# Kernel tuning notes

Measured on AMD Instinct MI355X. Metric: run time of the kernel, lower is better.

## Reference

```python
import jax, jax.numpy as jnp
import numpy as np

B, N, DIM = 32, 577, 768   # N = num_patches + 1
H, DH = 12, 64             # heads, dim_head; inner_dim = H*DH = 768
NEG = -987654321.0         # LSA diagonal mask value from the source


def setup_inputs() -> dict:
    key = jax.random.key(0)
    ks = jax.random.split(key, 5)
    inner = H * DH
    base_scale = DH ** -0.5
    return {
        "x": jax.random.normal(ks[0], (B, N, DIM), dtype=jnp.float32),
        "W_qkv": jax.random.normal(ks[1], (DIM, inner * 3), dtype=jnp.float32) * (DIM ** -0.5),
        "scale": base_scale * (1.0 + 0.01 * jax.random.normal(ks[2], (H,), dtype=jnp.float32)),
        "W_out": jax.random.normal(ks[3], (inner, DIM), dtype=jnp.float32) * (inner ** -0.5),
        "b_out": jnp.zeros((DIM,), dtype=jnp.float32),
    }


def reference(x, W_qkv, scale, W_out, b_out):
    b, n, _ = x.shape
    qkv = x @ W_qkv                                   # [b, n, 3*H*DH]
    q, k, v = jnp.split(qkv, 3, axis=-1)
    to_heads = lambda t: t.reshape(b, n, H, DH).transpose(0, 2, 1, 3)  # b h n d
    q, k, v = to_heads(q), to_heads(k), to_heads(v)
    # per-head learnable scale (LSA)
    dots = jnp.einsum('bhid,bhjd->bhij', q, k) * scale[None, :, None, None]
    # mask self-attention diagonal (eye scatter in the torch source)
    eye = jnp.eye(n, dtype=bool)
    dots = jnp.where(eye[None, None], NEG, dots)
    attn = jax.nn.softmax(dots, axis=-1)
    out = jnp.einsum('bhij,bhjd->bhid', attn, v)      # b h n d
    out = out.transpose(0, 2, 1, 3).reshape(b, n, H * DH)
    return out @ W_out + b_out
```

## Files before the change

kernel.cpp:

```cpp
#include <hip/hip_runtime.h>


typedef _Float16 half8  __attribute__((ext_vector_type(8)));
typedef _Float16 h4f    __attribute__((ext_vector_type(4)));
typedef __fp16   hv2    __attribute__((ext_vector_type(2)));
typedef __fp16   hv4    __attribute__((ext_vector_type(4)));
typedef float    floatx4 __attribute__((ext_vector_type(4)));

#define MTOT   18464
#define NEG_V  (-987654321.0f)
#define VTS    584

__device__ __forceinline__ void gl_lds16(const _Float16* g, _Float16* l) {
    __builtin_amdgcn_global_load_lds(
        (const __attribute__((address_space(1))) unsigned int*)g,
        (__attribute__((address_space(3))) unsigned int*)l,
        16, 0, 0);
}

__global__ __launch_bounds__(256) void cvt_x(const float* __restrict__ x,
                                             _Float16* __restrict__ x16) {
    const size_t idx = ((size_t)blockIdx.x * 256 + threadIdx.x) * 8;
    half8 h = {};
    if (idx < (size_t)MTOT * 768) {
        float4 a = *(const float4*)(x + idx);
        float4 b = *(const float4*)(x + idx + 4);
        h[0] = (_Float16)a.x; h[1] = (_Float16)a.y;
        h[2] = (_Float16)a.z; h[3] = (_Float16)a.w;
        h[4] = (_Float16)b.x; h[5] = (_Float16)b.y;
        h[6] = (_Float16)b.z; h[7] = (_Float16)b.w;
    }
    *(half8*)(x16 + idx) = h;
}

__global__ __launch_bounds__(256) void transpose_w(const float* __restrict__ src,
                                                   _Float16* __restrict__ dst,
                                                   int K, int Ncol) {
    __shared__ float tile[32][33];
    const int n0 = blockIdx.x * 32, k0 = blockIdx.y * 32;
    const int tx = threadIdx.x & 31, ty = threadIdx.x >> 5;
    for (int i = 0; i < 32; i += 8)
        tile[ty + i][tx] = src[(size_t)(k0 + ty + i) * Ncol + (n0 + tx)];
    __syncthreads();
    for (int i = 0; i < 32; i += 8)
        dst[(size_t)(n0 + ty + i) * K + (k0 + tx)] = (_Float16)tile[tx][ty + i];
}

__global__ __launch_bounds__(512, 4) void gemm_qkv(const _Float16* __restrict__ x16,
                                                   const _Float16* __restrict__ wT,
                                                   const float* __restrict__ scale,
                                                   _Float16* __restrict__ qg,
                                                   _Float16* __restrict__ kg,
                                                   _Float16* __restrict__ vT) {
    __shared__ _Float16 As[2][128 * 32];
    __shared__ _Float16 Bs[2][256 * 32];
    const unsigned orig = blockIdx.x;
    const unsigned xcd = orig & 7u, bidx = orig >> 3;
    const unsigned swz = (xcd == 0u ? 0u : 164u + (xcd - 1u) * 163u) + bidx;
    const unsigned mi = swz / 9u, ni = swz - mi * 9u;
    const int m0 = (int)mi * 128, n0 = (int)ni * 256;
    const int tid = threadIdx.x;
    const int lane = tid & 63, wv = tid >> 6;
    const int wrow = wv >> 2, wcol = wv & 3;
    const int lr = lane & 15, lq = lane >> 4;

    const int ra  = tid >> 2,         ca  = (((tid & 3) ^ ((ra  >> 1) & 3)) * 8);
    const int rb0 = tid >> 2,         cb0 = (((tid & 3) ^ ((rb0 >> 1) & 3)) * 8);
    const int rb1 = (512 + tid) >> 2, cb1 = (((tid & 3) ^ ((rb1 >> 1) & 3)) * 8);
    const int xc = (lq ^ ((lr >> 1) & 3)) * 8;

    floatx4 acc[4][4];
    const floatx4 fz = {0.f, 0.f, 0.f, 0.f};
    for (int i = 0; i < 4; ++i)
        for (int j = 0; j < 4; ++j) acc[i][j] = fz;

    #define STAGE_QKV(ki, bfx)                                                     \
        do {                                                                       \
            const int kk_ = (ki) * 32;                                             \
            gl_lds16(x16 + (size_t)(m0 + ra) * 768 + kk_ + ca, &As[bfx][wv*64*8]); \
            gl_lds16(wT + (size_t)(n0 + rb0) * 768 + kk_ + cb0, &Bs[bfx][wv*64*8]);\
            gl_lds16(wT + (size_t)(n0 + rb1) * 768 + kk_ + cb1,                    \
                     &Bs[bfx][(512 + wv*64) * 8]);                                 \
        } while (0)

    STAGE_QKV(0, 0);
    for (int ki = 0; ki < 24; ++ki) {
        const int bf = ki & 1;
        if (ki < 23) {
            STAGE_QKV(ki + 1, bf ^ 1);
            asm volatile("s_waitcnt vmcnt(3)" ::: "memory");
        } else {
            asm volatile("s_waitcnt vmcnt(0)" ::: "memory");
        }
        asm volatile("s_barrier" ::: "memory");

        half8 af[4], bfr[4];
        #pragma unroll
        for (int i = 0; i < 4; ++i)
            af[i] = *(const half8*)&As[bf][(wrow * 64 + i * 16 + lr) * 32 + xc];
        #pragma unroll
        for (int j = 0; j < 4; ++j)
            bfr[j] = *(const half8*)&Bs[bf][(wcol * 64 + j * 16 + lr) * 32 + xc];
        #pragma unroll
        for (int i = 0; i < 4; ++i)
            #pragma unroll
            for (int j = 0; j < 4; ++j)
                acc[i][j] = __builtin_amdgcn_mfma_f32_16x16x32_f16(af[i], bfr[j], acc[i][j], 0, 0, 0);

        asm volatile("s_waitcnt lgkmcnt(0)\n\ts_barrier" ::: "memory");
    }
    #undef STAGE_QKV

    const int cbase = n0 + wcol * 64;
    const int which = cbase / 768;
    const int h = (cbase - which * 768) >> 6;
    const float qsc = (which == 0) ? scale[h] * 1.4426950408889634f : 1.0f;
    #pragma unroll
    for (int j = 0; j < 4; ++j) {
        const int d = j * 16 + lr;
        #pragma unroll
        for (int i = 0; i < 4; ++i)
            #pragma unroll
            for (int r = 0; r < 4; ++r) {
                const int row = m0 + wrow * 64 + i * 16 + lq * 4 + r;
                if (row >= MTOT) continue;
                const unsigned bb = (unsigned)row / 577u;
                const unsigned nn = (unsigned)row - bb * 577u;
                const _Float16 val = (_Float16)(acc[i][j][r] * qsc);
                const size_t head = (size_t)(bb * 12 + h);
                if (which == 0)      qg[(head * 577 + nn) * 64 + d] = val;
                else if (which == 1) kg[(head * 577 + nn) * 64 + d] = val;
                else                 vT[(head * 64 + d) * VTS + nn] = val;
            }
    }
}

__global__ __launch_bounds__(256) void attn_kernel(const _Float16* __restrict__ qg,
                                                   const _Float16* __restrict__ kg,
                                                   const _Float16* __restrict__ vT,
                                                   _Float16* __restrict__ Og) {
    __shared__ __align__(16) _Float16 Ks[64 * 64];
    __shared__ __align__(16) _Float16 Vs[64 * 64];
    const unsigned orig = blockIdx.x;
    const unsigned swz = (orig & 7u) * 240u + (orig >> 3);
    const int qt = (int)(swz % 5u);
    const unsigned hb = swz / 5u;
    const int h = (int)(hb % 12u), b = (int)(hb / 12u);
    const int tid = threadIdx.x, lane = tid & 63, wv = tid >> 6;
    const int lr = lane & 15, lq = lane >> 4;
    const size_t head = (size_t)(b * 12 + h);
    const _Float16* qh = qg + head * 577 * 64;
    const _Float16* kh = kg + head * 577 * 64;
    const _Float16* vh = vT + head * 64 * VTS;
    const int q0 = qt * 128;
    const int xs = lq ^ (lr & 7), xs4 = xs ^ 4;

    half8 bq[2][2];
    #pragma unroll
    for (int st = 0; st < 2; ++st) {
        const int qi = q0 + st * 64 + wv * 16 + lr;
        const int qc = qi < 577 ? qi : 576;
        bq[st][0] = *(const half8*)(qh + (size_t)qc * 64 + lq * 8);
        bq[st][1] = *(const half8*)(qh + (size_t)qc * 64 + 32 + lq * 8);
    }

    const floatx4 fz = {0.f, 0.f, 0.f, 0.f};
    floatx4 ot[2][4];
    #pragma unroll
    for (int st = 0; st < 2; ++st)
        #pragma unroll
        for (int c = 0; c < 4; ++c) ot[st][c] = fz;
    float sacc[2] = {0.f, 0.f};

    for (int kt = 0; kt < 10; ++kt) {
        const int j0 = kt * 64;
        __syncthreads();
        #pragma unroll
        for (int t = 0; t < 2; ++t) {
            const int c = t * 256 + wv * 64 + lane;
            const int row = c >> 3, cl = (c & 7) ^ (row & 7);
            gl_lds16(kh + (size_t)(j0 + row) * 64 + cl * 8,
                     Ks + (t * 256 + wv * 64) * 8);
            gl_lds16(vh + (size_t)row * VTS + j0 + cl * 8,
                     Vs + (t * 256 + wv * 64) * 8);
        }
        __syncthreads();

        half8 ak[4][2];
        #pragma unroll
        for (int ct = 0; ct < 4; ++ct) {
            const int base = (ct * 16 + lr) * 64;
            ak[ct][0] = *(const half8*)&Ks[base + xs * 8];
            ak[ct][1] = *(const half8*)&Ks[base + xs4 * 8];
        }

        floatx4 s[2][4];
        __builtin_amdgcn_s_setprio(1);
        #pragma unroll
        for (int st = 0; st < 2; ++st)
            #pragma unroll
            for (int ct = 0; ct < 4; ++ct) {
                floatx4 t = __builtin_amdgcn_mfma_f32_16x16x32_f16(ak[ct][0], bq[st][0], fz, 0, 0, 0);
                s[st][ct] = __builtin_amdgcn_mfma_f32_16x16x32_f16(ak[ct][1], bq[st][1], t, 0, 0, 0);
            }
        __builtin_amdgcn_s_setprio(0);

        if (kt == 9) {
            #pragma unroll
            for (int st = 0; st < 2; ++st) {
                s[st][0][0] = (lq == 0) ? s[st][0][0] : -INFINITY;
                s[st][0][1] = -INFINITY; s[st][0][2] = -INFINITY; s[st][0][3] = -INFINITY;
                #pragma unroll
                for (int ct = 1; ct < 4; ++ct) {
                    s[st][ct][0] = -INFINITY; s[st][ct][1] = -INFINITY;
                    s[st][ct][2] = -INFINITY; s[st][ct][3] = -INFINITY;
                }
            }
        }
        #pragma unroll
        for (int st = 0; st < 2; ++st) {
            if (kt == qt * 2 + st) {
                #pragma unroll
                for (int ct = 0; ct < 4; ++ct)
                    if (ct == wv) {
                        #pragma unroll
                        for (int r = 0; r < 4; ++r)
                            if (lq * 4 + r == lr) s[st][ct][r] = -INFINITY;
                    }
            }
        }

        hv4 pk[2][4];
        #pragma unroll
        for (int st = 0; st < 2; ++st)
            #pragma unroll
            for (int ct = 0; ct < 4; ++ct) {
                const float p0 = __builtin_amdgcn_exp2f(s[st][ct][0]);
                const float p1 = __builtin_amdgcn_exp2f(s[st][ct][1]);
                const float p2 = __builtin_amdgcn_exp2f(s[st][ct][2]);
                const float p3 = __builtin_amdgcn_exp2f(s[st][ct][3]);
                sacc[st] += (p0 + p1) + (p2 + p3);
                const hv2 lo = __builtin_amdgcn_cvt_pkrtz(p0, p1);
                const hv2 hi = __builtin_amdgcn_cvt_pkrtz(p2, p3);
                pk[st][ct] = __builtin_shufflevector(lo, hi, 0, 1, 2, 3);
            }

        __builtin_amdgcn_s_setprio(1);
        #pragma unroll
        for (int jc = 0; jc < 4; ++jc) {
            const int csv = ((jc << 1) | (lq >> 1)) ^ (lr & 7);
            #pragma unroll
            for (int ctd = 0; ctd < 4; ++ctd) {
                const hv4 av = *(const hv4*)&Vs[(ctd * 16 + lr) * 64 + csv * 8 + (lq & 1) * 4];
                #pragma unroll
                for (int st = 0; st < 2; ++st)
                    ot[st][ctd] = __builtin_amdgcn_mfma_f32_16x16x16f16(av, pk[st][jc], ot[st][ctd], 0, 0, 0);
            }
        }
        __builtin_amdgcn_s_setprio(0);
    }

    #pragma unroll
    for (int st = 0; st < 2; ++st) {
        float l = sacc[st];
        l += __shfl_xor(l, 16, 64);
        l += __shfl_xor(l, 32, 64);
        const float linv = 1.f / l;
        const int i = q0 + st * 64 + wv * 16 + lr;
        if (i < 577) {
            #pragma unroll
            for (int ctd = 0; ctd < 4; ++ctd) {
                h4f ov;
                #pragma unroll
                for (int r = 0; r < 4; ++r) ov[r] = (_Float16)(ot[st][ctd][r] * linv);
                *(h4f*)(Og + ((size_t)(b * 577 + i)) * 768 + h * 64 + ctd * 16 + lq * 4) = ov;
            }
        }
    }
}

__global__ __launch_bounds__(512, 4) void gemm_out(const _Float16* __restrict__ Og,
                                                   const _Float16* __restrict__ wT,
                                                   const float* __restrict__ bias,
                                                   float* __restrict__ out) {
    __shared__ _Float16 As[2][128 * 32];
    __shared__ _Float16 Bs[2][256 * 32];
    const unsigned orig = blockIdx.x;
    const unsigned xcd = orig & 7u, bidx = orig >> 3;
    const unsigned swz = (xcd < 3u ? xcd * 55u : 165u + (xcd - 3u) * 54u) + bidx;
    const unsigned mi = swz / 3u, ni = swz - mi * 3u;
    const int m0 = (int)mi * 128, n0 = (int)ni * 256;
    const int tid = threadIdx.x;
    const int lane = tid & 63, wv = tid >> 6;
    const int wrow = wv >> 2, wcol = wv & 3;
    const int lr = lane & 15, lq = lane >> 4;

    const int ra  = tid >> 2,         ca  = (((tid & 3) ^ ((ra  >> 1) & 3)) * 8);
    const int rb0 = tid >> 2,         cb0 = (((tid & 3) ^ ((rb0 >> 1) & 3)) * 8);
    const int rb1 = (512 + tid) >> 2, cb1 = (((tid & 3) ^ ((rb1 >> 1) & 3)) * 8);
    const int xc = (lq ^ ((lr >> 1) & 3)) * 8;

    floatx4 acc[4][4];
    const floatx4 fz = {0.f, 0.f, 0.f, 0.f};
    for (int i = 0; i < 4; ++i)
        for (int j = 0; j < 4; ++j) acc[i][j] = fz;

    #define STAGE_OUT(ki, bfx)                                                     \
        do {                                                                       \
            const int kk_ = (ki) * 32;                                             \
            gl_lds16(Og + (size_t)(m0 + ra) * 768 + kk_ + ca, &As[bfx][wv*64*8]);  \
            gl_lds16(wT + (size_t)(n0 + rb0) * 768 + kk_ + cb0, &Bs[bfx][wv*64*8]);\
            gl_lds16(wT + (size_t)(n0 + rb1) * 768 + kk_ + cb1,                    \
                     &Bs[bfx][(512 + wv*64) * 8]);                                 \
        } while (0)

    STAGE_OUT(0, 0);
    for (int ki = 0; ki < 24; ++ki) {
        const int bf = ki & 1;
        if (ki < 23) {
            STAGE_OUT(ki + 1, bf ^ 1);
            asm volatile("s_waitcnt vmcnt(3)" ::: "memory");
        } else {
            asm volatile("s_waitcnt vmcnt(0)" ::: "memory");
        }
        asm volatile("s_barrier" ::: "memory");

        half8 af[4], bfr[4];
        #pragma unroll
        for (int i = 0; i < 4; ++i)
            af[i] = *(const half8*)&As[bf][(wrow * 64 + i * 16 + lr) * 32 + xc];
        #pragma unroll
        for (int j = 0; j < 4; ++j)
            bfr[j] = *(const half8*)&Bs[bf][(wcol * 64 + j * 16 + lr) * 32 + xc];
        #pragma unroll
        for (int i = 0; i < 4; ++i)
            #pragma unroll
            for (int j = 0; j < 4; ++j)
                acc[i][j] = __builtin_amdgcn_mfma_f32_16x16x32_f16(af[i], bfr[j], acc[i][j], 0, 0, 0);

        asm volatile("s_waitcnt lgkmcnt(0)\n\ts_barrier" ::: "memory");
    }
    #undef STAGE_OUT

    #pragma unroll
    for (int j = 0; j < 4; ++j) {
        const int c = n0 + wcol * 64 + j * 16 + lr;
        const float bv = bias[c];
        #pragma unroll
        for (int i = 0; i < 4; ++i)
            #pragma unroll
            for (int r = 0; r < 4; ++r) {
                const int row = m0 + wrow * 64 + i * 16 + lq * 4 + r;
                if (row < MTOT) out[(size_t)row * 768 + c] = acc[i][j][r] + bv;
            }
    }
}

extern "C" void kernel_launch(void* const* d_in, const int* in_sizes, int n_in,
                              void* d_out, int out_size, void* d_ws, size_t ws_size,
                              hipStream_t stream) {
    const float* x      = (const float*)d_in[0];
    const float* W_qkv  = (const float*)d_in[1];
    const float* scale  = (const float*)d_in[2];
    const float* W_out  = (const float*)d_in[3];
    const float* b_out  = (const float*)d_in[4];
    float* out = (float*)d_out;

    char* ws = (char*)d_ws;
    _Float16* x16   = (_Float16*)(ws);
    _Float16* Og    = x16;
    _Float16* qg    = (_Float16*)(ws + 28508160u);
    _Float16* kg    = (_Float16*)(ws + 28508160u + 28360704u);
    _Float16* vT    = (_Float16*)(ws + 28508160u + 2u * 28360704u);
    _Float16* WqkvT = (_Float16*)(ws + 28508160u + 2u * 28360704u + 28704768u);
    _Float16* WoutT = WqkvT + (size_t)2304 * 768;

    cvt_x<<<6960, 256, 0, stream>>>(x, x16);
    transpose_w<<<dim3(72, 24), 256, 0, stream>>>(W_qkv, WqkvT, 768, 2304);
    transpose_w<<<dim3(24, 24), 256, 0, stream>>>(W_out, WoutT, 768, 768);
    gemm_qkv<<<1305, 512, 0, stream>>>(x16, WqkvT, scale, qg, kg, vT);
    attn_kernel<<<1920, 256, 0, stream>>>(qg, kg, vT, Og);
    gemm_out<<<435, 512, 0, stream>>>(Og, WoutT, b_out, out);
}
```

Before: 358.4 us.

## Shrink GEMM tiles to 128x128 with 256-thread blocks and drop attention setprio

Both projection GEMMs go from 128x256 tiles with 8 waves to 128x128 tiles with 4 waves. This doubles the grid, and the XCD swizzle, load staging and vmcnt counts are rewritten to match. The aim is better wave balance across CUs and more concurrent blocks, at the cost of less B-tile reuse per block and more global traffic. Separately, the s_setprio calls around the attention MFMA sections are removed.

```diff
diff --git a/kernel.cpp b/kernel.cpp
--- a/kernel.cpp
+++ b/kernel.cpp
@@ -46,27 +46,26 @@
         dst[(size_t)(n0 + ty + i) * K + (k0 + tx)] = (_Float16)tile[tx][ty + i];
 }
 
-__global__ __launch_bounds__(512, 4) void gemm_qkv(const _Float16* __restrict__ x16,
+__global__ __launch_bounds__(256, 4) void gemm_qkv(const _Float16* __restrict__ x16,
                                                    const _Float16* __restrict__ wT,
                                                    const float* __restrict__ scale,
                                                    _Float16* __restrict__ qg,
                                                    _Float16* __restrict__ kg,
                                                    _Float16* __restrict__ vT) {
     __shared__ _Float16 As[2][128 * 32];
-    __shared__ _Float16 Bs[2][256 * 32];
+    __shared__ _Float16 Bs[2][128 * 32];
     const unsigned orig = blockIdx.x;
     const unsigned xcd = orig & 7u, bidx = orig >> 3;
-    const unsigned swz = (xcd == 0u ? 0u : 164u + (xcd - 1u) * 163u) + bidx;
-    const unsigned mi = swz / 9u, ni = swz - mi * 9u;
-    const int m0 = (int)mi * 128, n0 = (int)ni * 256;
+    const unsigned swz = (xcd < 2u ? xcd * 327u : 654u + (xcd - 2u) * 326u) + bidx;
+    const unsigned mi = swz / 18u, ni = swz - mi * 18u;
+    const int m0 = (int)mi * 128, n0 = (int)ni * 128;
     const int tid = threadIdx.x;
     const int lane = tid & 63, wv = tid >> 6;
-    const int wrow = wv >> 2, wcol = wv & 3;
+    const int wrow = wv >> 1, wcol = wv & 1;
     const int lr = lane & 15, lq = lane >> 4;
 
-    const int ra  = tid >> 2,         ca  = (((tid & 3) ^ ((ra  >> 1) & 3)) * 8);
-    const int rb0 = tid >> 2,         cb0 = (((tid & 3) ^ ((rb0 >> 1) & 3)) * 8);
-    const int rb1 = (512 + tid) >> 2, cb1 = (((tid & 3) ^ ((rb1 >> 1) & 3)) * 8);
+    const int r1 = tid >> 2,        c1 = (((tid & 3) ^ ((r1 >> 1) & 3)) * 8);
+    const int r2 = 64 + (tid >> 2), c2 = (((tid & 3) ^ ((r2 >> 1) & 3)) * 8);
     const int xc = (lq ^ ((lr >> 1) & 3)) * 8;
 
     floatx4 acc[4][4];
@@ -74,13 +73,15 @@
     for (int i = 0; i < 4; ++i)
         for (int j = 0; j < 4; ++j) acc[i][j] = fz;
 
-    #define STAGE_QKV(ki, bfx)                                                     \
-        do {                                                                       \
-            const int kk_ = (ki) * 32;                                             \
-            gl_lds16(x16 + (size_t)(m0 + ra) * 768 + kk_ + ca, &As[bfx][wv*64*8]); \
-            gl_lds16(wT + (size_t)(n0 + rb0) * 768 + kk_ + cb0, &Bs[bfx][wv*64*8]);\
-            gl_lds16(wT + (size_t)(n0 + rb1) * 768 + kk_ + cb1,                    \
-                     &Bs[bfx][(512 + wv*64) * 8]);                                 \
+    #define STAGE_QKV(ki, bfx)                                                      \
+        do {                                                                        \
+            const int kk_ = (ki) * 32;                                              \
+            gl_lds16(x16 + (size_t)(m0 + r1) * 768 + kk_ + c1, &As[bfx][wv*64*8]);  \
+            gl_lds16(x16 + (size_t)(m0 + r2) * 768 + kk_ + c2,                      \
+                     &As[bfx][(256 + wv*64) * 8]);                                  \
+            gl_lds16(wT + (size_t)(n0 + r1) * 768 + kk_ + c1, &Bs[bfx][wv*64*8]);   \
+            gl_lds16(wT + (size_t)(n0 + r2) * 768 + kk_ + c2,                       \
+                     &Bs[bfx][(256 + wv*64) * 8]);                                  \
         } while (0)
 
     STAGE_QKV(0, 0);
@@ -88,7 +89,7 @@
         const int bf = ki & 1;
         if (ki < 23) {
             STAGE_QKV(ki + 1, bf ^ 1);
-            asm volatile("s_waitcnt vmcnt(3)" ::: "memory");
+            asm volatile("s_waitcnt vmcnt(4)" ::: "memory");
         } else {
             asm volatile("s_waitcnt vmcnt(0)" ::: "memory");
         }
@@ -195,7 +196,6 @@
         }
 
         floatx4 s[2][4];
-        __builtin_amdgcn_s_setprio(1);
         #pragma unroll
         for (int st = 0; st < 2; ++st)
             #pragma unroll
@@ -203,7 +203,6 @@
                 floatx4 t = __builtin_amdgcn_mfma_f32_16x16x32_f16(ak[ct][0], bq[st][0], fz, 0, 0, 0);
                 s[st][ct] = __builtin_amdgcn_mfma_f32_16x16x32_f16(ak[ct][1], bq[st][1], t, 0, 0, 0);
             }
-        __builtin_amdgcn_s_setprio(0);
 
         if (kt == 9) {
             #pragma unroll
@@ -245,7 +244,6 @@
                 pk[st][ct] = __builtin_shufflevector(lo, hi, 0, 1, 2, 3);
             }
 
-        __builtin_amdgcn_s_setprio(1);
         #pragma unroll
         for (int jc = 0; jc < 4; ++jc) {
             const int csv = ((jc << 1) | (lq >> 1)) ^ (lr & 7);
@@ -257,7 +255,6 @@
                     ot[st][ctd] = __builtin_amdgcn_mfma_f32_16x16x16f16(av, pk[st][jc], ot[st][ctd], 0, 0, 0);
             }
         }
-        __builtin_amdgcn_s_setprio(0);
     }
 
     #pragma unroll
@@ -279,25 +276,24 @@
     }
 }
 
-__global__ __launch_bounds__(512, 4) void gemm_out(const _Float16* __restrict__ Og,
+__global__ __launch_bounds__(256, 4) void gemm_out(const _Float16* __restrict__ Og,
                                                    const _Float16* __restrict__ wT,
                                                    const float* __restrict__ bias,
                                                    float* __restrict__ out) {
     __shared__ _Float16 As[2][128 * 32];
-    __shared__ _Float16 Bs[2][256 * 32];
+    __shared__ _Float16 Bs[2][128 * 32];
     const unsigned orig = blockIdx.x;
     const unsigned xcd = orig & 7u, bidx = orig >> 3;
-    const unsigned swz = (xcd < 3u ? xcd * 55u : 165u + (xcd - 3u) * 54u) + bidx;
-    const unsigned mi = swz / 3u, ni = swz - mi * 3u;
-    const int m0 = (int)mi * 128, n0 = (int)ni * 256;
+    const unsigned swz = (xcd < 6u ? xcd * 109u : 654u + (xcd - 6u) * 108u) + bidx;
+    const unsigned mi = swz / 6u, ni = swz - mi * 6u;
+    const int m0 = (int)mi * 128, n0 = (int)ni * 128;
     const int tid = threadIdx.x;
     const int lane = tid & 63, wv = tid >> 6;
-    const int wrow = wv >> 2, wcol = wv & 3;
+    const int wrow = wv >> 1, wcol = wv & 1;
     const int lr = lane & 15, lq = lane >> 4;
 
-    const int ra  = tid >> 2,         ca  = (((tid & 3) ^ ((ra  >> 1) & 3)) * 8);
-    const int rb0 = tid >> 2,         cb0 = (((tid & 3) ^ ((rb0 >> 1) & 3)) * 8);
-    const int rb1 = (512 + tid) >> 2, cb1 = (((tid & 3) ^ ((rb1 >> 1) & 3)) * 8);
+    const int r1 = tid >> 2,        c1 = (((tid & 3) ^ ((r1 >> 1) & 3)) * 8);
+    const int r2 = 64 + (tid >> 2), c2 = (((tid & 3) ^ ((r2 >> 1) & 3)) * 8);
     const int xc = (lq ^ ((lr >> 1) & 3)) * 8;
 
     floatx4 acc[4][4];
@@ -305,13 +301,15 @@
     for (int i = 0; i < 4; ++i)
         for (int j = 0; j < 4; ++j) acc[i][j] = fz;
 
-    #define STAGE_OUT(ki, bfx)                                                     \
-        do {                                                                       \
-            const int kk_ = (ki) * 32;                                             \
-            gl_lds16(Og + (size_t)(m0 + ra) * 768 + kk_ + ca, &As[bfx][wv*64*8]);  \
-            gl_lds16(wT + (size_t)(n0 + rb0) * 768 + kk_ + cb0, &Bs[bfx][wv*64*8]);\
-            gl_lds16(wT + (size_t)(n0 + rb1) * 768 + kk_ + cb1,                    \
-                     &Bs[bfx][(512 + wv*64) * 8]);                                 \
+    #define STAGE_OUT(ki, bfx)                                                      \
+        do {                                                                        \
+            const int kk_ = (ki) * 32;                                              \
+            gl_lds16(Og + (size_t)(m0 + r1) * 768 + kk_ + c1, &As[bfx][wv*64*8]);   \
+            gl_lds16(Og + (size_t)(m0 + r2) * 768 + kk_ + c2,                       \
+                     &As[bfx][(256 + wv*64) * 8]);                                  \
+            gl_lds16(wT + (size_t)(n0 + r1) * 768 + kk_ + c1, &Bs[bfx][wv*64*8]);   \
+            gl_lds16(wT + (size_t)(n0 + r2) * 768 + kk_ + c2,                       \
+                     &Bs[bfx][(256 + wv*64) * 8]);                                  \
         } while (0)
 
     STAGE_OUT(0, 0);
@@ -319,7 +317,7 @@
         const int bf = ki & 1;
         if (ki < 23) {
             STAGE_OUT(ki + 1, bf ^ 1);
-            asm volatile("s_waitcnt vmcnt(3)" ::: "memory");
+            asm volatile("s_waitcnt vmcnt(4)" ::: "memory");
         } else {
             asm volatile("s_waitcnt vmcnt(0)" ::: "memory");
         }
@@ -378,7 +376,7 @@
     cvt_x<<<6960, 256, 0, stream>>>(x, x16);
     transpose_w<<<dim3(72, 24), 256, 0, stream>>>(W_qkv, WqkvT, 768, 2304);
     transpose_w<<<dim3(24, 24), 256, 0, stream>>>(W_out, WoutT, 768, 768);
-    gemm_qkv<<<1305, 512, 0, stream>>>(x16, WqkvT, scale, qg, kg, vT);
+    gemm_qkv<<<2610, 256, 0, stream>>>(x16, WqkvT, scale, qg, kg, vT);
     attn_kernel<<<1920, 256, 0, stream>>>(qg, kg, vT, Og);
-    gemm_out<<<435, 512, 0, stream>>>(Og, WoutT, b_out, out);
-}
+    gemm_out<<<870, 256, 0, stream>>>(Og, WoutT, b_out, out);
+}
```

Measured after the change: 355.1 us. About the same (-0.9%).
